# Optimization experiments

Hardware: AMD Instinct MI355X
Metric: run time of the kernel (lower is better)

Reference implementation:

```python
import jax, jax.numpy as jnp
import numpy as np

TANH_CONST = 2.5
TEMPERATURE = 5.0


def setup_inputs() -> dict:
    key = jax.random.key(0)
    ks = jax.random.split(key, 9)
    B, L, NB, H, NC = 16384, 64, 8, 128, 1000
    return {
        "class_ids": jax.random.randint(ks[0], (B,), 0, NC),
        "gumbel_u": jax.random.uniform(ks[1], (L, B, NB), dtype=jnp.float32),
        "g_emb": jax.random.normal(ks[2], (NC, H), dtype=jnp.float32) * 0.1,
        "w_emb": jax.random.normal(ks[3], (NB, H), dtype=jnp.float32) * 0.1,
        "w_soft": jax.random.normal(ks[4], (NB, H), dtype=jnp.float32) * 0.1,
        "w_ih": jax.random.normal(ks[5], (4 * H, H), dtype=jnp.float32) * 0.1,
        "w_hh": jax.random.normal(ks[6], (4 * H, H), dtype=jnp.float32) * 0.1,
        "b_ih": jax.random.normal(ks[7], (4 * H,), dtype=jnp.float32) * 0.1,
        "b_hh": jax.random.normal(ks[8], (4 * H,), dtype=jnp.float32) * 0.1,
    }


def reference(class_ids, gumbel_u, g_emb, w_emb, w_soft, w_ih, w_hh, b_ih, b_hh):
    B = class_ids.shape[0]
    H = g_emb.shape[1]
    x0 = g_emb[class_ids]                      # [B, H] class embedding (reused each step)
    h0 = jnp.zeros((B, H), x0.dtype)
    c0 = jnp.zeros((B, H), x0.dtype)

    def step(carry, u):
        h, c, x = carry
        gates = x @ w_ih.T + h @ w_hh.T + b_ih + b_hh   # [B, 4H], torch gate order i,f,g,o
        i, f, g, o = jnp.split(gates, 4, axis=-1)
        c2 = jax.nn.sigmoid(f) * c + jax.nn.sigmoid(i) * jnp.tanh(g)
        h2 = jax.nn.sigmoid(o) * jnp.tanh(c2)
        logit = h2 @ w_soft.T                           # [B, NB]
        logit = TANH_CONST * jnp.tanh(logit / TEMPERATURE)
        # categorical sample via gumbel-max
        uc = jnp.clip(u, 1e-8, 1.0 - 1e-8)
        gmb = -jnp.log(-jnp.log(uc))
        branch = jnp.argmax(logit + gmb, axis=-1)       # [B] int
        logp = jax.nn.log_softmax(logit, axis=-1)
        lp = jnp.take_along_axis(logp, branch[:, None], axis=1)[:, 0]
        ent = -jnp.sum(jnp.exp(logp) * logp, axis=-1)
        x2 = (w_emb[branch] + x0) * 0.5
        return (h2, c2, x2), (branch, lp, ent)

    _, (arcs, lps, ents) = jax.lax.scan(step, (h0, c0, x0), gumbel_u)
    # stack along dim=1 like torch.stack(..., dim=1) -> [B, L]
    sample_arc = arcs.T
    sample_log_prob = lps.T
    sample_entropy = ents.T
    sample_prob = jnp.exp(sample_log_prob)
    return sample_arc, sample_log_prob, sample_entropy, sample_prob
```

## Files before the change

### kernel.cpp

```cpp
#include <hip/hip_runtime.h>
#include <math.h>

#define HD 128
#define NBR 8
#define LSTEPS 64
#define TILE_B 32
#define HT_PAD 36
#define PART_PAD 133

#define WPT_OFF   0
#define WIPT_OFF  65536
#define PP_OFF    131072
#define BSUM_OFF  135168

__global__ __launch_bounds__(256) void setup_kernel(
    const float* __restrict__ w_emb, const float* __restrict__ w_ih,
    const float* __restrict__ w_hh, const float* __restrict__ b_ih,
    const float* __restrict__ b_hh, float* __restrict__ ws)
{
  int tid = blockIdx.x * blockDim.x + threadIdx.x;
  if (tid < 65536) {
    int k = tid >> 9, col = tid & 511;
    int hh = col >> 2, q = col & 3;
    ws[WPT_OFF + tid]  = w_hh[(q*HD + hh)*HD + k];
    ws[WIPT_OFF + tid] = w_ih[(q*HD + hh)*HD + k];
  }
  if (tid < 4096) {
    int j = tid >> 9, rem = tid & 511;
    int q = rem >> 7, hh2 = rem & 127;
    const float* wr = w_ih + (q*HD + hh2)*HD;
    const float* er = w_emb + j*HD;
    float s = 0.f;
    for (int k = 0; k < HD; ++k) s = fmaf(er[k], wr[k], s);
    ws[PP_OFF + (size_t)j*512 + q*HD + hh2] = s + b_ih[q*HD + hh2] + b_hh[q*HD + hh2];
  }
  if (tid < 512) {
    int q = tid >> 7, hh2 = tid & 127;
    ws[BSUM_OFF + tid] = b_ih[q*HD + hh2] + b_hh[q*HD + hh2];
  }
}

__global__ __launch_bounds__(512, 4) void ctrl_kernel(
    const int* __restrict__ class_ids,
    const float* __restrict__ gumbel_u,
    const float* __restrict__ g_emb,
    const float* __restrict__ w_soft,
    const float* __restrict__ ws,
    float* __restrict__ out,
    int Btot)
{
  __shared__ float hT[HD * HT_PAD];
  __shared__ float wsoft_l[NBR * HD];
  __shared__ float part_l[TILE_B * PART_PAD];
  __shared__ float pp_l[NBR * 512];
  __shared__ int   br_l[TILE_B];

  const int tid = threadIdx.x;
  const int b0  = blockIdx.x * TILE_B;
  const size_t BL = (size_t)Btot * LSTEPS;

  const float* __restrict__ wpT  = ws + WPT_OFF;
  const float* __restrict__ wipT = ws + WIPT_OFF;

  for (int i = tid; i < NBR*HD; i += 512) wsoft_l[i] = w_soft[i];
  for (int i = tid; i < NBR*512; i += 512) pp_l[i] = ws[PP_OFF + i];

  const int hh = tid & 127;
  const int bg = tid >> 7;

  {
    int sb = tid >> 4;
    int kc = tid & 15;
    int cid = class_ids[b0 + sb];
    const float* src = g_emb + (size_t)cid * HD + kc*8;
    float4 v0 = *(const float4*)(src);
    float4 v1 = *(const float4*)(src + 4);
    int kb = kc*8;
    hT[(kb+0)*HT_PAD + sb] = v0.x;
    hT[(kb+1)*HT_PAD + sb] = v0.y;
    hT[(kb+2)*HT_PAD + sb] = v0.z;
    hT[(kb+3)*HT_PAD + sb] = v0.w;
    hT[(kb+4)*HT_PAD + sb] = v1.x;
    hT[(kb+5)*HT_PAD + sb] = v1.y;
    hT[(kb+6)*HT_PAD + sb] = v1.z;
    hT[(kb+7)*HT_PAD + sb] = v1.w;
  }
  __syncthreads();

  float q0[4][8];
  #pragma unroll
  for (int q = 0; q < 4; ++q)
    #pragma unroll
    for (int j = 0; j < 8; ++j) q0[q][j] = 0.f;

  {
    const float* wp = wipT + 4*hh;
    const float* hr = &hT[bg*8];
    #pragma unroll 2
    for (int k = 0; k < HD; ++k) {
      float4 w  = *(const float4*)(wp);
      float4 ha = *(const float4*)(hr);
      float4 hb = *(const float4*)(hr + 4);
      wp += 512; hr += HT_PAD;
      float hv[8] = {ha.x,ha.y,ha.z,ha.w,hb.x,hb.y,hb.z,hb.w};
      float wv[4] = {w.x,w.y,w.z,w.w};
      #pragma unroll
      for (int q = 0; q < 4; ++q)
        #pragma unroll
        for (int j = 0; j < 8; ++j)
          q0[q][j] = fmaf(hv[j], wv[q], q0[q][j]);
    }
  }
  #pragma unroll
  for (int q = 0; q < 4; ++q) {
    float bs = ws[BSUM_OFF + q*HD + hh];
    #pragma unroll
    for (int j = 0; j < 8; ++j) q0[q][j] += bs;
  }
  __syncthreads();

  float c[8];
  #pragma unroll
  for (int j = 0; j < 8; ++j) c[j] = 0.f;

  for (int t = 0; t < LSTEPS; ++t) {
    float4 ua = make_float4(0,0,0,0), ub = make_float4(0,0,0,0);
    if (tid < TILE_B) {
      const float* up = gumbel_u + ((size_t)t * Btot + (b0 + tid)) * NBR;
      ua = *(const float4*)up;
      ub = *(const float4*)(up + 4);
    }

    float acc[4][8];
    #pragma unroll
    for (int q = 0; q < 4; ++q)
      #pragma unroll
      for (int j = 0; j < 8; ++j) acc[q][j] = 0.f;

    if (t > 0) {
      const float* wp = wpT + 4*hh;
      const float* hr = &hT[bg*8];
      #pragma unroll 2
      for (int k = 0; k < HD; ++k) {
        float4 w  = *(const float4*)(wp);
        float4 ha = *(const float4*)(hr);
        float4 hb = *(const float4*)(hr + 4);
        wp += 512; hr += HT_PAD;
        float hv[8] = {ha.x,ha.y,ha.z,ha.w,hb.x,hb.y,hb.z,hb.w};
        float wv[4] = {w.x,w.y,w.z,w.w};
        #pragma unroll
        for (int q = 0; q < 4; ++q)
          #pragma unroll
          for (int j = 0; j < 8; ++j)
            acc[q][j] = fmaf(hv[j], wv[q], acc[q][j]);
      }
    }

    float h2v[8];
    #pragma unroll
    for (int j = 0; j < 8; ++j) {
      float g4[4];
      if (t == 0) {
        #pragma unroll
        for (int q = 0; q < 4; ++q) g4[q] = q0[q][j];
      } else {
        int br = br_l[bg*8 + j];
        const float* pr = pp_l + br*512 + hh;
        #pragma unroll
        for (int q = 0; q < 4; ++q)
          g4[q] = fmaf(0.5f, pr[q*HD] + q0[q][j], acc[q][j]);
      }
      float iv = 1.f/(1.f + expf(-g4[0]));
      float fv = 1.f/(1.f + expf(-g4[1]));
      float gv = tanhf(g4[2]);
      float ov = 1.f/(1.f + expf(-g4[3]));
      float c2 = fv*c[j] + iv*gv;
      c[j] = c2;
      h2v[j] = ov * tanhf(c2);
    }
    __syncthreads();

    {
      float* dst = &hT[hh*HT_PAD + bg*8];
      *(float4*)(dst)   = make_float4(h2v[0],h2v[1],h2v[2],h2v[3]);
      *(float4*)(dst+4) = make_float4(h2v[4],h2v[5],h2v[6],h2v[7]);
    }
    __syncthreads();

    {
      int lb = tid & 31, ch = tid >> 5;
      float part[8];
      #pragma unroll
      for (int nb = 0; nb < 8; ++nb) part[nb] = 0.f;
      #pragma unroll
      for (int i = 0; i < 8; ++i) {
        float hvv = hT[(ch*8 + i)*HT_PAD + lb];
        #pragma unroll
        for (int nb = 0; nb < 8; ++nb)
          part[nb] = fmaf(hvv, wsoft_l[nb*HD + ch*8 + i], part[nb]);
      }
      #pragma unroll
      for (int nb = 0; nb < 8; ++nb)
        part_l[lb*PART_PAD + nb*16 + ch] = part[nb];
    }
    __syncthreads();

    if (tid < TILE_B) {
      int lb = tid;
      float lg[8];
      #pragma unroll
      for (int nb = 0; nb < 8; ++nb) {
        float s = 0.f;
        #pragma unroll
        for (int ch = 0; ch < 16; ++ch) s += part_l[lb*PART_PAD + nb*16 + ch];
        lg[nb] = 2.5f * tanhf(s / 5.0f);
      }
      float uv[8] = {ua.x,ua.y,ua.z,ua.w,ub.x,ub.y,ub.z,ub.w};
      int br = 0; float best;
      {
        float uc = fminf(fmaxf(uv[0], 1e-8f), 0.99999999f);
        best = lg[0] - logf(-logf(uc));
      }
      #pragma unroll
      for (int nb = 1; nb < 8; ++nb) {
        float uc = fminf(fmaxf(uv[nb], 1e-8f), 0.99999999f);
        float y = lg[nb] - logf(-logf(uc));
        if (y > best) { best = y; br = nb; }
      }
      float m = lg[0];
      #pragma unroll
      for (int nb = 1; nb < 8; ++nb) m = fmaxf(m, lg[nb]);
      float se = 0.f;
      #pragma unroll
      for (int nb = 0; nb < 8; ++nb) se += expf(lg[nb] - m);
      float lse = logf(se);
      float lp = (lg[br] - m) - lse;
      float ent = 0.f;
      #pragma unroll
      for (int nb = 0; nb < 8; ++nb) {
        float lpi = (lg[nb] - m) - lse;
        ent -= expf(lpi) * lpi;
      }
      size_t row = (size_t)(b0 + lb) * LSTEPS + t;
      out[row]        = (float)br;
      out[BL + row]   = lp;
      out[2*BL + row] = ent;
      out[3*BL + row] = expf(lp);
      br_l[lb] = br;
    }
    __syncthreads();
  }
}

extern "C" void kernel_launch(void* const* d_in, const int* in_sizes, int n_in,
                              void* d_out, int out_size, void* d_ws, size_t ws_size,
                              hipStream_t stream) {
  const int*   class_ids = (const int*)d_in[0];
  const float* gumbel_u  = (const float*)d_in[1];
  const float* g_emb     = (const float*)d_in[2];
  const float* w_emb     = (const float*)d_in[3];
  const float* w_soft    = (const float*)d_in[4];
  const float* w_ih      = (const float*)d_in[5];
  const float* w_hh      = (const float*)d_in[6];
  const float* b_ih      = (const float*)d_in[7];
  const float* b_hh      = (const float*)d_in[8];
  float* out = (float*)d_out;
  float* ws  = (float*)d_ws;
  int B = in_sizes[0];

  hipLaunchKernelGGL(setup_kernel, dim3(256), dim3(256), 0, stream,
                     w_emb, w_ih, w_hh, b_ih, b_hh, ws);
  hipLaunchKernelGGL(ctrl_kernel, dim3(B / TILE_B), dim3(512), 0, stream,
                     class_ids, gumbel_u, g_emb, w_soft, ws, out, B);
}
```

Baseline: 2.340 ms.

## Double-buffer hidden state, park input gates in AGPRs, use fast math intrinsics

The hidden-state tile is now double-buffered across two shared arrays, which removes one barrier per timestep. The precomputed input-gate contribution is kept in accumulator registers through inline asm to relieve VGPR pressure. The branch-embedding gate table is re-laid out so four gates load as one float4, and gumbel noise is computed before the matmul. Sigmoid, tanh, exp and log switch to fast intrinsics, and the softmax-projection inner loops are restructured for vectorized LDS reads, trading some numerical precision for fewer instructions.

```diff
diff --git a/kernel.cpp b/kernel.cpp
--- a/kernel.cpp
+++ b/kernel.cpp
@@ -6,7 +6,7 @@
 #define LSTEPS 64
 #define TILE_B 32
 #define HT_PAD 36
-#define PART_PAD 133
+#define PART_PAD 132
 
 #define WPT_OFF   0
 #define WIPT_OFF  65536
@@ -32,13 +32,36 @@
     const float* er = w_emb + j*HD;
     float s = 0.f;
     for (int k = 0; k < HD; ++k) s = fmaf(er[k], wr[k], s);
-    ws[PP_OFF + (size_t)j*512 + q*HD + hh2] = s + b_ih[q*HD + hh2] + b_hh[q*HD + hh2];
+    ws[PP_OFF + (size_t)j*512 + 4*hh2 + q] = s + b_ih[q*HD + hh2] + b_hh[q*HD + hh2];
   }
   if (tid < 512) {
     int q = tid >> 7, hh2 = tid & 127;
     ws[BSUM_OFF + tid] = b_ih[q*HD + hh2] + b_hh[q*HD + hh2];
   }
 }
+
+__device__ __forceinline__ float fsig(float x) {
+  return __fdividef(1.f, 1.f + __expf(-x));
+}
+__device__ __forceinline__ float ftanh(float x) {
+  float ax = fabsf(x);
+  float e  = __expf(-2.f * ax);
+  float r  = __fdividef(1.f - e, 1.f + e);
+  return copysignf(r, x);
+}
+
+#define ROWQ(qi, wq) \
+  acc[qi][0] = fmaf(ha.x, wq, acc[qi][0]); acc[qi][1] = fmaf(ha.y, wq, acc[qi][1]); \
+  acc[qi][2] = fmaf(ha.z, wq, acc[qi][2]); acc[qi][3] = fmaf(ha.w, wq, acc[qi][3]); \
+  acc[qi][4] = fmaf(hb.x, wq, acc[qi][4]); acc[qi][5] = fmaf(hb.y, wq, acc[qi][5]); \
+  acc[qi][6] = fmaf(hb.z, wq, acc[qi][6]); acc[qi][7] = fmaf(hb.w, wq, acc[qi][7]);
+
+#define KSTEP(WPTR, HPTR) do { \
+    float4 w  = *(const float4*)(WPTR); \
+    float4 ha = *(const float4*)(HPTR); \
+    float4 hb = *(const float4*)((HPTR) + 4); \
+    ROWQ(0, w.x) ROWQ(1, w.y) ROWQ(2, w.z) ROWQ(3, w.w) \
+  } while (0)
 
 __global__ __launch_bounds__(512, 4) void ctrl_kernel(
     const int* __restrict__ class_ids,
@@ -49,11 +72,12 @@
     float* __restrict__ out,
     int Btot)
 {
-  __shared__ float hT[HD * HT_PAD];
-  __shared__ float wsoft_l[NBR * HD];
-  __shared__ float part_l[TILE_B * PART_PAD];
-  __shared__ float pp_l[NBR * 512];
-  __shared__ int   br_l[TILE_B];
+  __shared__ __align__(16) float hT0[HD * HT_PAD];
+  __shared__ __align__(16) float hT1[HD * HT_PAD];
+  __shared__ __align__(16) float wsoft_l[NBR * HD];
+  __shared__ __align__(16) float part_l[TILE_B * PART_PAD];
+  __shared__ __align__(16) float pp_l[NBR * 512];
+  __shared__ int br_l[TILE_B];
 
   const int tid = threadIdx.x;
   const int b0  = blockIdx.x * TILE_B;
@@ -76,46 +100,41 @@
     float4 v0 = *(const float4*)(src);
     float4 v1 = *(const float4*)(src + 4);
     int kb = kc*8;
-    hT[(kb+0)*HT_PAD + sb] = v0.x;
-    hT[(kb+1)*HT_PAD + sb] = v0.y;
-    hT[(kb+2)*HT_PAD + sb] = v0.z;
-    hT[(kb+3)*HT_PAD + sb] = v0.w;
-    hT[(kb+4)*HT_PAD + sb] = v1.x;
-    hT[(kb+5)*HT_PAD + sb] = v1.y;
-    hT[(kb+6)*HT_PAD + sb] = v1.z;
-    hT[(kb+7)*HT_PAD + sb] = v1.w;
+    hT0[(kb+0)*HT_PAD + sb] = v0.x;
+    hT0[(kb+1)*HT_PAD + sb] = v0.y;
+    hT0[(kb+2)*HT_PAD + sb] = v0.z;
+    hT0[(kb+3)*HT_PAD + sb] = v0.w;
+    hT0[(kb+4)*HT_PAD + sb] = v1.x;
+    hT0[(kb+5)*HT_PAD + sb] = v1.y;
+    hT0[(kb+6)*HT_PAD + sb] = v1.z;
+    hT0[(kb+7)*HT_PAD + sb] = v1.w;
   }
   __syncthreads();
 
-  float q0[4][8];
-  #pragma unroll
-  for (int q = 0; q < 4; ++q)
-    #pragma unroll
-    for (int j = 0; j < 8; ++j) q0[q][j] = 0.f;
-
+  float qpark[32];
   {
-    const float* wp = wipT + 4*hh;
-    const float* hr = &hT[bg*8];
+    float acc[4][8];
+    #pragma unroll
+    for (int q = 0; q < 4; ++q)
+      #pragma unroll
+      for (int j = 0; j < 8; ++j) acc[q][j] = 0.f;
+
+    const float* wrow = wipT + 4*hh;
+    const float* hr   = hT0 + bg*8;
     #pragma unroll 2
     for (int k = 0; k < HD; ++k) {
-      float4 w  = *(const float4*)(wp);
-      float4 ha = *(const float4*)(hr);
-      float4 hb = *(const float4*)(hr + 4);
-      wp += 512; hr += HT_PAD;
-      float hv[8] = {ha.x,ha.y,ha.z,ha.w,hb.x,hb.y,hb.z,hb.w};
-      float wv[4] = {w.x,w.y,w.z,w.w};
-      #pragma unroll
-      for (int q = 0; q < 4; ++q)
-        #pragma unroll
-        for (int j = 0; j < 8; ++j)
-          q0[q][j] = fmaf(hv[j], wv[q], q0[q][j]);
-    }
-  }
-  #pragma unroll
-  for (int q = 0; q < 4; ++q) {
-    float bs = ws[BSUM_OFF + q*HD + hh];
-    #pragma unroll
-    for (int j = 0; j < 8; ++j) q0[q][j] += bs;
+      KSTEP(wrow, hr);
+      wrow += 512; hr += HT_PAD;
+    }
+    #pragma unroll
+    for (int q = 0; q < 4; ++q) {
+      float bs = ws[BSUM_OFF + q*HD + hh];
+      #pragma unroll
+      for (int j = 0; j < 8; ++j) {
+        float v = 0.5f * (acc[q][j] + bs);
+        asm("v_accvgpr_write_b32 %0, %1" : "=a"(qpark[q*8+j]) : "v"(v));
+      }
+    }
   }
   __syncthreads();
 
@@ -123,65 +142,68 @@
   #pragma unroll
   for (int j = 0; j < 8; ++j) c[j] = 0.f;
 
+  float* hcur = hT0;
+  float* hnxt = hT1;
+
   for (int t = 0; t < LSTEPS; ++t) {
-    float4 ua = make_float4(0,0,0,0), ub = make_float4(0,0,0,0);
+    float gmb[8];
     if (tid < TILE_B) {
       const float* up = gumbel_u + ((size_t)t * Btot + (b0 + tid)) * NBR;
-      ua = *(const float4*)up;
-      ub = *(const float4*)(up + 4);
+      float4 ua = *(const float4*)up;
+      float4 ub = *(const float4*)(up + 4);
+      float uv[8] = {ua.x,ua.y,ua.z,ua.w,ub.x,ub.y,ub.z,ub.w};
+      #pragma unroll
+      for (int nb = 0; nb < 8; ++nb) {
+        float uc = fminf(fmaxf(uv[nb], 1e-8f), 0.99999999f);
+        gmb[nb] = -__logf(-__logf(uc));
+      }
     }
 
     float acc[4][8];
     #pragma unroll
     for (int q = 0; q < 4; ++q)
       #pragma unroll
-      for (int j = 0; j < 8; ++j) acc[q][j] = 0.f;
+      for (int j = 0; j < 8; ++j)
+        asm("v_accvgpr_read_b32 %0, %1" : "=v"(acc[q][j]) : "a"(qpark[q*8+j]));
 
     if (t > 0) {
-      const float* wp = wpT + 4*hh;
-      const float* hr = &hT[bg*8];
+      __builtin_amdgcn_s_setprio(1);
+      const float* wrow = wpT + 4*hh;
+      const float* hr   = hcur + bg*8;
       #pragma unroll 2
       for (int k = 0; k < HD; ++k) {
-        float4 w  = *(const float4*)(wp);
-        float4 ha = *(const float4*)(hr);
-        float4 hb = *(const float4*)(hr + 4);
-        wp += 512; hr += HT_PAD;
-        float hv[8] = {ha.x,ha.y,ha.z,ha.w,hb.x,hb.y,hb.z,hb.w};
-        float wv[4] = {w.x,w.y,w.z,w.w};
-        #pragma unroll
-        for (int q = 0; q < 4; ++q)
-          #pragma unroll
-          for (int j = 0; j < 8; ++j)
-            acc[q][j] = fmaf(hv[j], wv[q], acc[q][j]);
-      }
+        KSTEP(wrow, hr);
+        wrow += 512; hr += HT_PAD;
+      }
+      __builtin_amdgcn_s_setprio(0);
     }
 
     float h2v[8];
     #pragma unroll
     for (int j = 0; j < 8; ++j) {
-      float g4[4];
+      float gi, gf, gg, go;
       if (t == 0) {
-        #pragma unroll
-        for (int q = 0; q < 4; ++q) g4[q] = q0[q][j];
+        gi = 2.f*acc[0][j]; gf = 2.f*acc[1][j];
+        gg = 2.f*acc[2][j]; go = 2.f*acc[3][j];
       } else {
         int br = br_l[bg*8 + j];
-        const float* pr = pp_l + br*512 + hh;
-        #pragma unroll
-        for (int q = 0; q < 4; ++q)
-          g4[q] = fmaf(0.5f, pr[q*HD] + q0[q][j], acc[q][j]);
-      }
-      float iv = 1.f/(1.f + expf(-g4[0]));
-      float fv = 1.f/(1.f + expf(-g4[1]));
-      float gv = tanhf(g4[2]);
-      float ov = 1.f/(1.f + expf(-g4[3]));
-      float c2 = fv*c[j] + iv*gv;
+        float4 pv = *(const float4*)(&pp_l[br*512 + 4*hh]);
+        gi = fmaf(0.5f, pv.x, acc[0][j]);
+        gf = fmaf(0.5f, pv.y, acc[1][j]);
+        gg = fmaf(0.5f, pv.z, acc[2][j]);
+        go = fmaf(0.5f, pv.w, acc[3][j]);
+      }
+      float iv = fsig(gi);
+      float fv = fsig(gf);
+      float gv = ftanh(gg);
+      float ov = fsig(go);
+      float c2 = fmaf(fv, c[j], iv*gv);
       c[j] = c2;
-      h2v[j] = ov * tanhf(c2);
-    }
-    __syncthreads();
+      h2v[j] = ov * ftanh(c2);
+    }
 
     {
-      float* dst = &hT[hh*HT_PAD + bg*8];
+      float* dst = &hnxt[hh*HT_PAD + bg*8];
       *(float4*)(dst)   = make_float4(h2v[0],h2v[1],h2v[2],h2v[3]);
       *(float4*)(dst+4) = make_float4(h2v[4],h2v[5],h2v[6],h2v[7]);
     }
@@ -189,19 +211,21 @@
 
     {
       int lb = tid & 31, ch = tid >> 5;
-      float part[8];
-      #pragma unroll
-      for (int nb = 0; nb < 8; ++nb) part[nb] = 0.f;
-      #pragma unroll
-      for (int i = 0; i < 8; ++i) {
-        float hvv = hT[(ch*8 + i)*HT_PAD + lb];
-        #pragma unroll
-        for (int nb = 0; nb < 8; ++nb)
-          part[nb] = fmaf(hvv, wsoft_l[nb*HD + ch*8 + i], part[nb]);
-      }
-      #pragma unroll
-      for (int nb = 0; nb < 8; ++nb)
-        part_l[lb*PART_PAD + nb*16 + ch] = part[nb];
+      const float* hp = hnxt + (ch*8)*HT_PAD + lb;
+      float hv[8];
+      #pragma unroll
+      for (int i = 0; i < 8; ++i) hv[i] = hp[i*HT_PAD];
+      #pragma unroll
+      for (int nb = 0; nb < 8; ++nb) {
+        const float4* wr = (const float4*)&wsoft_l[nb*HD + ch*8];
+        float4 wa = wr[0], wb = wr[1];
+        float p = 0.f;
+        p = fmaf(hv[0], wa.x, p); p = fmaf(hv[1], wa.y, p);
+        p = fmaf(hv[2], wa.z, p); p = fmaf(hv[3], wa.w, p);
+        p = fmaf(hv[4], wb.x, p); p = fmaf(hv[5], wb.y, p);
+        p = fmaf(hv[6], wb.z, p); p = fmaf(hv[7], wb.w, p);
+        part_l[lb*PART_PAD + nb*16 + ch] = p;
+      }
     }
     __syncthreads();
 
@@ -210,45 +234,44 @@
       float lg[8];
       #pragma unroll
       for (int nb = 0; nb < 8; ++nb) {
-        float s = 0.f;
-        #pragma unroll
-        for (int ch = 0; ch < 16; ++ch) s += part_l[lb*PART_PAD + nb*16 + ch];
-        lg[nb] = 2.5f * tanhf(s / 5.0f);
-      }
-      float uv[8] = {ua.x,ua.y,ua.z,ua.w,ub.x,ub.y,ub.z,ub.w};
-      int br = 0; float best;
-      {
-        float uc = fminf(fmaxf(uv[0], 1e-8f), 0.99999999f);
-        best = lg[0] - logf(-logf(uc));
-      }
+        const float4* pr = (const float4*)&part_l[lb*PART_PAD + nb*16];
+        float4 pa = pr[0], pb = pr[1], pc = pr[2], pd = pr[3];
+        float s = pa.x; s += pa.y; s += pa.z; s += pa.w;
+        s += pb.x; s += pb.y; s += pb.z; s += pb.w;
+        s += pc.x; s += pc.y; s += pc.z; s += pc.w;
+        s += pd.x; s += pd.y; s += pd.z; s += pd.w;
+        lg[nb] = 2.5f * ftanh(s * 0.2f);
+      }
+      int br = 0; float best = lg[0] + gmb[0];
       #pragma unroll
       for (int nb = 1; nb < 8; ++nb) {
-        float uc = fminf(fmaxf(uv[nb], 1e-8f), 0.99999999f);
-        float y = lg[nb] - logf(-logf(uc));
+        float y = lg[nb] + gmb[nb];
         if (y > best) { best = y; br = nb; }
       }
+      br_l[lb] = br;
       float m = lg[0];
       #pragma unroll
       for (int nb = 1; nb < 8; ++nb) m = fmaxf(m, lg[nb]);
       float se = 0.f;
       #pragma unroll
-      for (int nb = 0; nb < 8; ++nb) se += expf(lg[nb] - m);
-      float lse = logf(se);
+      for (int nb = 0; nb < 8; ++nb) se += __expf(lg[nb] - m);
+      float lse = __logf(se);
       float lp = (lg[br] - m) - lse;
-      float ent = 0.f;
-      #pragma unroll
-      for (int nb = 0; nb < 8; ++nb) {
-        float lpi = (lg[nb] - m) - lse;
-        ent -= expf(lpi) * lpi;
-      }
       size_t row = (size_t)(b0 + lb) * LSTEPS + t;
       out[row]        = (float)br;
       out[BL + row]   = lp;
+      out[3*BL + row] = __expf(lp);
+      float ent = 0.f;
+      #pragma unroll
+      for (int nb = 0; nb < 8; ++nb) {
+        float lpi = (lg[nb] - m) - lse;
+        ent -= __expf(lpi) * lpi;
+      }
       out[2*BL + row] = ent;
-      out[3*BL + row] = expf(lp);
-      br_l[lb] = br;
     }
     __syncthreads();
+
+    float* tmp = hcur; hcur = hnxt; hnxt = tmp;
   }
 }
 
```

After: 2.080 ms. 1.12x faster.
